# Optimization experiments

Hardware: AMD Instinct MI355X
Metric: run time of the kernel (lower is better)

The kernel has to match this reference:

```python
import jax, jax.numpy as jnp
import numpy as np

N_NODES = 100000
N_EDGES = 1600000
N_GRAPHS = 64
IN_DIM = 397


def setup_inputs() -> dict:
    key = jax.random.key(0)
    ks = jax.random.split(key, 16)
    x = jax.random.normal(ks[0], (N_NODES, IN_DIM), dtype=jnp.float32)
    edge_index = jax.random.randint(ks[1], (2, N_EDGES), 0, N_NODES, dtype=jnp.int64)
    batch = jnp.sort(jax.random.randint(ks[2], (N_NODES,), 0, N_GRAPHS, dtype=jnp.int64))

    def lin(k, fan_in, fan_out):
        s = 1.0 / np.sqrt(fan_in)
        return jax.random.uniform(k, (fan_in, fan_out), jnp.float32, -s, s)

    return {
        "x": x, "edge_index": edge_index, "batch": batch,
        "W1": lin(ks[3], IN_DIM, 128), "b1": jnp.zeros((128,), jnp.float32),
        "W2": lin(ks[4], 128, 128),   "b2": jnp.zeros((128,), jnp.float32),
        "W3": lin(ks[5], 128, 64),    "b3": jnp.zeros((64,), jnp.float32),
        "Wh1": lin(ks[6], 64, 32),    "bh1": jnp.zeros((32,), jnp.float32),
        "Wh2": lin(ks[7], 32, 1),     "bh2": jnp.zeros((1,), jnp.float32),
    }


def _gcn_conv(x, src, dst, deg_isqrt, W, b, n_nodes):
    # PyG GCNConv: linear first, then sym-normalized aggregation with self-loops.
    xw = x @ W  # [N, out]
    norm = deg_isqrt[src] * deg_isqrt[dst]  # [E]
    agg = jax.ops.segment_sum(xw[src] * norm[:, None], dst, num_segments=n_nodes)
    # self-loop contribution: deg^{-1/2}[i] * deg^{-1/2}[i] * xw[i]
    agg = agg + xw * (deg_isqrt * deg_isqrt)[:, None]
    return agg + b


def reference(x, edge_index, batch, W1, b1, W2, b2, W3, b3, Wh1, bh1, Wh2, bh2):
    n_nodes = x.shape[0]
    src, dst = edge_index[0], edge_index[1]
    # degree after adding self-loops (edge weight 1), counted at destination
    deg = jax.ops.segment_sum(jnp.ones_like(src, dtype=x.dtype), dst,
                              num_segments=n_nodes) + 1.0
    deg_isqrt = jax.lax.rsqrt(deg)

    h = jax.nn.relu(_gcn_conv(x, src, dst, deg_isqrt, W1, b1, n_nodes))
    # dropout p=0.2 -> identity in eval
    h = jax.nn.relu(_gcn_conv(h, src, dst, deg_isqrt, W2, b2, n_nodes))
    h = jax.nn.relu(_gcn_conv(h, src, dst, deg_isqrt, W3, b3, n_nodes))

    # global max pool over graphs in the batch
    g = jax.ops.segment_max(h, batch, num_segments=N_GRAPHS)  # [G, 64]

    # MLP head (Dropout(0.3) identity in eval)
    g = jax.nn.relu(g @ Wh1 + bh1)
    out = g @ Wh2 + bh2  # [G, 1]
    return out.squeeze(-1)
```

## Files before the change

kernel.cpp:

```cpp
#include <hip/hip_runtime.h>
#include <hip/hip_bf16.h>
#include <hip/hip_fp16.h>


typedef float f4u __attribute__((ext_vector_type(4), aligned(4)));
typedef unsigned short u16;
typedef u16 u16x8 __attribute__((ext_vector_type(8)));
typedef short bf16x8 __attribute__((ext_vector_type(8)));
typedef float f32x4 __attribute__((ext_vector_type(4)));
typedef _Float16 f16;
typedef f16 f16x8 __attribute__((ext_vector_type(8)));

__device__ __forceinline__ u16 bf16_rne(float f) {
    unsigned u = __float_as_uint(f);
    return (u16)((u + 0x7FFF + ((u >> 16) & 1)) >> 16);
}
__device__ __forceinline__ float bf16_f(u16 h) {
    return __uint_as_float(((unsigned)h) << 16);
}

__global__ void deg_count_kernel(const int* __restrict__ ei, int* __restrict__ cnt, int E) {
    int e = blockIdx.x * 256 + threadIdx.x;
    if (e < E) atomicAdd(&cnt[ei[E + e]], 1);
}

__global__ void deg_fin_kernel(const int* __restrict__ cnt, float* __restrict__ disq, int N) {
    int i = blockIdx.x * 256 + threadIdx.x;
    if (i < N) disq[i] = rsqrtf((float)cnt[i] + 1.0f);
}

__global__ void scan_pass1(const int* __restrict__ cnt, int* __restrict__ bsum, int N) {
    __shared__ int s[256];
    int t = threadIdx.x;
    int base = blockIdx.x * 1024 + t * 4;
    int sum = 0;
    #pragma unroll
    for (int j = 0; j < 4; ++j) { int idx = base + j; if (idx < N) sum += cnt[idx]; }
    s[t] = sum; __syncthreads();
    for (int off = 128; off; off >>= 1) {
        if (t < off) s[t] += s[t + off];
        __syncthreads();
    }
    if (t == 0) bsum[blockIdx.x] = s[0];
}

__global__ void scan_pass2(const int* __restrict__ bsum, int* __restrict__ boff,
                           int nchunks, int* __restrict__ rp, int N, int E) {
    __shared__ int s[256];
    int t = threadIdx.x;
    int v = (t < nchunks) ? bsum[t] : 0;
    s[t] = v; __syncthreads();
    for (int off = 1; off < 256; off <<= 1) {
        int x = (t >= off) ? s[t - off] : 0;
        __syncthreads();
        s[t] += x;
        __syncthreads();
    }
    boff[t] = s[t] - v;
    if (t == 0) rp[N] = E;
}

__global__ void scan_pass3(const int* __restrict__ cnt, const int* __restrict__ boff,
                           int* __restrict__ rp, int N) {
    __shared__ int s[256];
    int t = threadIdx.x;
    int base = blockIdx.x * 1024 + t * 4;
    int v[4]; int sum = 0;
    #pragma unroll
    for (int j = 0; j < 4; ++j) { int idx = base + j; v[j] = (idx < N) ? cnt[idx] : 0; sum += v[j]; }
    s[t] = sum; __syncthreads();
    for (int off = 1; off < 256; off <<= 1) {
        int x = (t >= off) ? s[t - off] : 0;
        __syncthreads();
        s[t] += x;
        __syncthreads();
    }
    int ex = s[t] - sum + boff[blockIdx.x];
    #pragma unroll
    for (int j = 0; j < 4; ++j) { int idx = base + j; if (idx < N) { rp[idx] = ex; ex += v[j]; } }
}

__global__ void scatter_kernel(const int* __restrict__ ei, const float* __restrict__ disq,
                               const int* __restrict__ rp, int* __restrict__ fill,
                               int2* __restrict__ esw, int E) {
    int e = blockIdx.x * 256 + threadIdx.x;
    if (e >= E) return;
    int s = ei[e];
    int d = ei[E + e];
    int pos = rp[d] + atomicAdd(&fill[d], 1);
    int2 p; p.x = s; p.y = __float_as_int(disq[s] * disq[d]);
    esw[pos] = p;
}

__global__ void cvtw_kernel(const float* __restrict__ W, u16* __restrict__ Wthi,
                            u16* __restrict__ Wtlo, int K, int KP, int BN) {
    int idx = blockIdx.x * 256 + threadIdx.x;
    if (idx >= KP * BN) return;
    int c = idx / KP;
    int k = idx % KP;
    float v = (k < K) ? W[(long)k * BN + c] : 0.f;
    u16 h = bf16_rne(v);
    Wthi[idx] = h;
    Wtlo[idx] = bf16_rne(v - bf16_f(h));
}

template <int BN, bool AFP32>
__global__ __launch_bounds__(512) void mfma_gemm(
    const float* __restrict__ Af, const u16* __restrict__ Ahi,
    const u16* __restrict__ Alo, const u16* __restrict__ Wthi,
    const u16* __restrict__ Wtlo, f16* __restrict__ Xh, int N, int K, int KP)
{
    constexpr int FC = BN / 16;
    __shared__ u16 Wh[BN * 40];
    __shared__ u16 Wl[BN * 40];
    const int tid = threadIdx.x;
    const int w = tid >> 6;
    const int l = tid & 63;
    const int l15 = l & 15;
    const int koff = (l >> 4) * 8;
    const long base = (long)blockIdx.x * 128;
    const long arow = base + w * 16 + l15;
    const bool rowOK = (arow < N);

    f32x4 acc[FC];
    #pragma unroll
    for (int j = 0; j < FC; ++j) acc[j] = (f32x4){0.f, 0.f, 0.f, 0.f};

    for (int k0 = 0; k0 < KP; k0 += 32) {
        {
            int i2 = tid;
            if (i2 < BN * 4) {
                int c = i2 >> 2;
                int kq = (i2 & 3) * 8;
                *(u16x8*)&Wh[c * 40 + kq] = *(const u16x8*)&Wthi[(long)c * KP + k0 + kq];
                *(u16x8*)&Wl[c * 40 + kq] = *(const u16x8*)&Wtlo[(long)c * KP + k0 + kq];
            }
        }
        bf16x8 ah, al;
        {
            u16x8 hv = (u16x8)0, lv = (u16x8)0;
            if constexpr (AFP32) {
                int rem = K - (k0 + koff);
                if (rowOK && rem > 0) {
                    const float* ap = &Af[arow * (long)K + k0 + koff];
                    float f[8];
                    if (rem >= 8) {
                        f4u v0 = *(const f4u*)ap;
                        f4u v1 = *(const f4u*)(ap + 4);
                        f[0] = v0.x; f[1] = v0.y; f[2] = v0.z; f[3] = v0.w;
                        f[4] = v1.x; f[5] = v1.y; f[6] = v1.z; f[7] = v1.w;
                    } else {
                        #pragma unroll
                        for (int j = 0; j < 8; ++j) f[j] = (j < rem) ? ap[j] : 0.f;
                    }
                    #pragma unroll
                    for (int j = 0; j < 8; ++j) {
                        u16 h = bf16_rne(f[j]);
                        hv[j] = h;
                        lv[j] = bf16_rne(f[j] - bf16_f(h));
                    }
                }
            } else {
                if (rowOK) {
                    hv = *(const u16x8*)&Ahi[arow * (long)K + k0 + koff];
                    lv = *(const u16x8*)&Alo[arow * (long)K + k0 + koff];
                }
            }
            ah = __builtin_bit_cast(bf16x8, hv);
            al = __builtin_bit_cast(bf16x8, lv);
        }
        __syncthreads();
        #pragma unroll
        for (int fc = 0; fc < FC; ++fc) {
            int wr = (fc * 16 + l15) * 40 + koff;
            bf16x8 bh = *(const bf16x8*)&Wh[wr];
            bf16x8 bl = *(const bf16x8*)&Wl[wr];
            acc[fc] = __builtin_amdgcn_mfma_f32_16x16x32_bf16(ah, bh, acc[fc], 0, 0, 0);
            acc[fc] = __builtin_amdgcn_mfma_f32_16x16x32_bf16(al, bh, acc[fc], 0, 0, 0);
            acc[fc] = __builtin_amdgcn_mfma_f32_16x16x32_bf16(ah, bl, acc[fc], 0, 0, 0);
        }
        __syncthreads();
    }
    #pragma unroll
    for (int fc = 0; fc < FC; ++fc) {
        int col = fc * 16 + l15;
        #pragma unroll
        for (int reg = 0; reg < 4; ++reg) {
            long row = base + w * 16 + (l >> 4) * 4 + reg;
            if (row < N) Xh[row * BN + col] = (f16)acc[fc][reg];
        }
    }
}

template <int C, bool B16OUT>
__global__ __launch_bounds__(256) void agg_kernel(
    const f16* __restrict__ xh, const float* __restrict__ disq,
    const int* __restrict__ rp, const int2* __restrict__ esw,
    const float* __restrict__ bias, float* __restrict__ h,
    u16* __restrict__ hhi, u16* __restrict__ hlo, int N)
{
    int i = blockIdx.x * 4 + (threadIdx.x >> 6);
    if (i >= N) return;
    int lane = threadIdx.x & 63;
    int e0 = rp[i], e1 = rp[i + 1];
    constexpr int LPE = C / 8;
    constexpr int EPW = 64 / LPE;
    int sub = lane / LPE;
    int col = lane % LPE;
    const f16x8* x8 = (const f16x8*)xh;

    float a0[8], a1[8];
    #pragma unroll
    for (int j = 0; j < 8; ++j) { a0[j] = 0.f; a1[j] = 0.f; }

    int e = e0 + sub;
    for (; e + EPW < e1; e += 2 * EPW) {
        int2 p0 = esw[e];
        int2 p1 = esw[e + EPW];
        f16x8 v0 = x8[(long)p0.x * LPE + col];
        f16x8 v1 = x8[(long)p1.x * LPE + col];
        float w0 = __int_as_float(p0.y), w1 = __int_as_float(p1.y);
        #pragma unroll
        for (int j = 0; j < 8; ++j) {
            a0[j] += (float)v0[j] * w0;
            a1[j] += (float)v1[j] * w1;
        }
    }
    for (; e < e1; e += EPW) {
        int2 p0 = esw[e];
        f16x8 v0 = x8[(long)p0.x * LPE + col];
        float w0 = __int_as_float(p0.y);
        #pragma unroll
        for (int j = 0; j < 8; ++j) a0[j] += (float)v0[j] * w0;
    }
    #pragma unroll
    for (int j = 0; j < 8; ++j) a0[j] += a1[j];
    #pragma unroll
    for (int m = LPE; m < 64; m <<= 1) {
        #pragma unroll
        for (int j = 0; j < 8; ++j) a0[j] += __shfl_xor(a0[j], m, 64);
    }
    if (sub == 0) {
        float ds = disq[i];
        float ws = ds * ds;
        f16x8 v = x8[(long)i * LPE + col];
        const float* bp = bias + col * 8;
        float4 b0 = *(const float4*)bp;
        float4 b1 = *(const float4*)(bp + 4);
        float bb[8] = {b0.x, b0.y, b0.z, b0.w, b1.x, b1.y, b1.z, b1.w};
        float o[8];
        #pragma unroll
        for (int j = 0; j < 8; ++j)
            o[j] = fmaxf(a0[j] + (float)v[j] * ws + bb[j], 0.f);
        if constexpr (B16OUT) {
            u16x8 oh, ol;
            #pragma unroll
            for (int j = 0; j < 8; ++j) {
                u16 hh = bf16_rne(o[j]);
                oh[j] = hh;
                ol[j] = bf16_rne(o[j] - bf16_f(hh));
            }
            *(u16x8*)&hhi[(long)i * C + col * 8] = oh;
            *(u16x8*)&hlo[(long)i * C + col * 8] = ol;
        } else {
            float4 v0 = {o[0], o[1], o[2], o[3]};
            float4 v1 = {o[4], o[5], o[6], o[7]};
            *(float4*)&h[(long)i * C + col * 8] = v0;
            *(float4*)&h[(long)i * C + col * 8 + 4] = v1;
        }
    }
}

__global__ __launch_bounds__(256) void pool_kernel(
    const float* __restrict__ h, const int* __restrict__ batch,
    float* __restrict__ g, int N)
{
    int c = threadIdx.x & 63;
    int slot = threadIdx.x >> 6;
    int base = blockIdx.x * 512;
    int end = base + 512; if (end > N) end = N;
    int cur = -1; float m = 0.f;
    for (int n = base + slot; n < end; n += 4) {
        int b = batch[n];
        float v = h[(long)n * 64 + c];
        if (b != cur) {
            if (cur >= 0) atomicMax((int*)&g[cur * 64 + c], __float_as_int(m));
            cur = b; m = v;
        } else {
            m = fmaxf(m, v);
        }
    }
    if (cur >= 0) atomicMax((int*)&g[cur * 64 + c], __float_as_int(m));
}

__global__ void head_kernel(const float* __restrict__ g, const float* __restrict__ Wh1,
                            const float* __restrict__ bh1, const float* __restrict__ Wh2,
                            const float* __restrict__ bh2, float* __restrict__ out, int G) {
    int r = threadIdx.x;
    if (r >= G) return;
    float hid[32];
    #pragma unroll
    for (int j = 0; j < 32; ++j) {
        float s = bh1[j];
        for (int k = 0; k < 64; ++k) s += g[r * 64 + k] * Wh1[k * 32 + j];
        hid[j] = fmaxf(s, 0.f);
    }
    float o = bh2[0];
    #pragma unroll
    for (int j = 0; j < 32; ++j) o += hid[j] * Wh2[j];
    out[r] = o;
}

extern "C" void kernel_launch(void* const* d_in, const int* in_sizes, int n_in,
                              void* d_out, int out_size, void* d_ws, size_t ws_size,
                              hipStream_t stream) {
    const float* x   = (const float*)d_in[0];
    const int*   ei  = (const int*)d_in[1];
    const int*   bat = (const int*)d_in[2];
    const float* W1  = (const float*)d_in[3];
    const float* b1  = (const float*)d_in[4];
    const float* W2  = (const float*)d_in[5];
    const float* b2  = (const float*)d_in[6];
    const float* W3  = (const float*)d_in[7];
    const float* b3  = (const float*)d_in[8];
    const float* Wh1 = (const float*)d_in[9];
    const float* bh1 = (const float*)d_in[10];
    const float* Wh2 = (const float*)d_in[11];
    const float* bh2 = (const float*)d_in[12];
    float* out = (float*)d_out;

    const int N = in_sizes[2];
    const int E = in_sizes[1] / 2;
    const int K1 = in_sizes[0] / N;
    const int G = out_size;
    const int KP1 = ((K1 + 31) / 32) * 32;

    char* wsp = (char*)d_ws;
    size_t off = 0;
    auto alloc = [&](size_t bytes) -> void* {
        void* p = wsp + off;
        off = (off + bytes + 255) & ~(size_t)255;
        return p;
    };
    int*   cnt   = (int*)alloc((size_t)N * 4);
    float* disq  = (float*)alloc((size_t)N * 4);
    int*   rp    = (int*)alloc((size_t)(N + 1) * 4);
    int*   bsum  = (int*)alloc(256 * 4);
    int*   boff  = (int*)alloc(256 * 4);
    int2*  esw   = (int2*)alloc((size_t)E * 8);
    u16*   Wt1hi = (u16*)alloc((size_t)KP1 * 128 * 2);
    u16*   Wt1lo = (u16*)alloc((size_t)KP1 * 128 * 2);
    u16*   Wt2hi = (u16*)alloc((size_t)128 * 128 * 2);
    u16*   Wt2lo = (u16*)alloc((size_t)128 * 128 * 2);
    u16*   Wt3hi = (u16*)alloc((size_t)128 * 64 * 2);
    u16*   Wt3lo = (u16*)alloc((size_t)128 * 64 * 2);
    f16*   Xh    = (f16*)alloc((size_t)N * 128 * 2);
    u16*   Hhi   = (u16*)alloc((size_t)N * 128 * 2);
    u16*   Hlo   = (u16*)alloc((size_t)N * 128 * 2);
    float* h3    = (float*)alloc((size_t)N * 64 * 4);
    float* g     = (float*)alloc((size_t)G * 64 * 4);

    const int nchunks = (N + 1023) / 1024;

    (void)hipMemsetAsync(cnt, 0, (size_t)N * 4, stream);
    deg_count_kernel<<<(E + 255) / 256, 256, 0, stream>>>(ei, cnt, E);
    deg_fin_kernel<<<(N + 255) / 256, 256, 0, stream>>>(cnt, disq, N);
    scan_pass1<<<nchunks, 256, 0, stream>>>(cnt, bsum, N);
    scan_pass2<<<1, 256, 0, stream>>>(bsum, boff, nchunks, rp, N, E);
    scan_pass3<<<nchunks, 256, 0, stream>>>(cnt, boff, rp, N);
    (void)hipMemsetAsync(cnt, 0, (size_t)N * 4, stream);
    scatter_kernel<<<(E + 255) / 256, 256, 0, stream>>>(ei, disq, rp, cnt, esw, E);

    cvtw_kernel<<<(KP1 * 128 + 255) / 256, 256, 0, stream>>>(W1, Wt1hi, Wt1lo, K1, KP1, 128);
    cvtw_kernel<<<(128 * 128 + 255) / 256, 256, 0, stream>>>(W2, Wt2hi, Wt2lo, 128, 128, 128);
    cvtw_kernel<<<(128 * 64 + 255) / 256, 256, 0, stream>>>(W3, Wt3hi, Wt3lo, 128, 128, 64);

    int gblocks = (N + 127) / 128;
    int ablocks = (N + 3) / 4;
    mfma_gemm<128, true><<<gblocks, 512, 0, stream>>>(x, nullptr, nullptr, Wt1hi, Wt1lo, Xh, N, K1, KP1);
    agg_kernel<128, true><<<ablocks, 256, 0, stream>>>(Xh, disq, rp, esw, b1, nullptr, Hhi, Hlo, N);
    mfma_gemm<128, false><<<gblocks, 512, 0, stream>>>(nullptr, Hhi, Hlo, Wt2hi, Wt2lo, Xh, N, 128, 128);
    agg_kernel<128, true><<<ablocks, 256, 0, stream>>>(Xh, disq, rp, esw, b2, nullptr, Hhi, Hlo, N);
    mfma_gemm<64, false><<<gblocks, 512, 0, stream>>>(nullptr, Hhi, Hlo, Wt3hi, Wt3lo, Xh, N, 128, 128);
    agg_kernel<64, false><<<ablocks, 256, 0, stream>>>(Xh, disq, rp, esw, b3, h3, nullptr, nullptr, N);
    (void)hipMemsetAsync(g, 0, (size_t)G * 64 * 4, stream);
    pool_kernel<<<(N + 511) / 512, 256, 0, stream>>>(h3, bat, g, N);
    head_kernel<<<1, 64, 0, stream>>>(g, Wh1, bh1, Wh2, bh2, out, G);
}
```

Baseline: 531.4 us.

## Retile MFMA GEMM to 64x32 per-wave tiles with weights read directly from global

Reworks the bf16x3 MFMA GEMM so each wave computes a 64-row by 32-column tile (4x2 fragments) instead of 16 rows by all columns. Weight fragments are loaded straight from global memory/cache into registers, and the shared-memory staging and both __syncthreads per K step are removed. The aim is to reuse each A fragment across two column fragments and each W fragment across four row fragments, and to drop the barrier stalls. In exchange, A rows are reread by several column-waves (BN=128 uses 4 waves per row block), register pressure goes up, and block size and grid change.

```diff
diff --git a/kernel.cpp b/kernel.cpp
--- a/kernel.cpp
+++ b/kernel.cpp
@@ -105,44 +105,46 @@
 }
 
 template <int BN, bool AFP32>
-__global__ __launch_bounds__(512) void mfma_gemm(
+__global__ __launch_bounds__(256) void mfma_gemm(
     const float* __restrict__ Af, const u16* __restrict__ Ahi,
     const u16* __restrict__ Alo, const u16* __restrict__ Wthi,
     const u16* __restrict__ Wtlo, f16* __restrict__ Xh, int N, int K, int KP)
 {
-    constexpr int FC = BN / 16;
-    __shared__ u16 Wh[BN * 40];
-    __shared__ u16 Wl[BN * 40];
+    constexpr int WCOL = BN / 32;
+    constexpr int BM = 64 * (4 / WCOL);
     const int tid = threadIdx.x;
     const int w = tid >> 6;
     const int l = tid & 63;
     const int l15 = l & 15;
     const int koff = (l >> 4) * 8;
-    const long base = (long)blockIdx.x * 128;
-    const long arow = base + w * 16 + l15;
-    const bool rowOK = (arow < N);
-
-    f32x4 acc[FC];
-    #pragma unroll
-    for (int j = 0; j < FC; ++j) acc[j] = (f32x4){0.f, 0.f, 0.f, 0.f};
-
+    const int cw = w % WCOL;
+    const int rw = w / WCOL;
+    const long base = (long)blockIdx.x * BM + rw * 64;
+
+    f32x4 acc[4][2];
+    #pragma unroll
+    for (int i = 0; i < 4; ++i)
+        #pragma unroll
+        for (int j = 0; j < 2; ++j) acc[i][j] = (f32x4){0.f, 0.f, 0.f, 0.f};
+
+    #pragma unroll 2
     for (int k0 = 0; k0 < KP; k0 += 32) {
-        {
-            int i2 = tid;
-            if (i2 < BN * 4) {
-                int c = i2 >> 2;
-                int kq = (i2 & 3) * 8;
-                *(u16x8*)&Wh[c * 40 + kq] = *(const u16x8*)&Wthi[(long)c * KP + k0 + kq];
-                *(u16x8*)&Wl[c * 40 + kq] = *(const u16x8*)&Wtlo[(long)c * KP + k0 + kq];
-            }
-        }
-        bf16x8 ah, al;
-        {
+        bf16x8 bh[2], bl[2];
+        #pragma unroll
+        for (int fc = 0; fc < 2; ++fc) {
+            long wr = (long)(cw * 32 + fc * 16 + l15) * KP + k0 + koff;
+            bh[fc] = __builtin_bit_cast(bf16x8, *(const u16x8*)(Wthi + wr));
+            bl[fc] = __builtin_bit_cast(bf16x8, *(const u16x8*)(Wtlo + wr));
+        }
+        bf16x8 ah[4], al[4];
+        #pragma unroll
+        for (int fr = 0; fr < 4; ++fr) {
+            long row = base + fr * 16 + l15;
             u16x8 hv = (u16x8)0, lv = (u16x8)0;
             if constexpr (AFP32) {
                 int rem = K - (k0 + koff);
-                if (rowOK && rem > 0) {
-                    const float* ap = &Af[arow * (long)K + k0 + koff];
+                if (row < N && rem > 0) {
+                    const float* ap = &Af[row * (long)K + k0 + koff];
                     float f[8];
                     if (rem >= 8) {
                         f4u v0 = *(const f4u*)ap;
@@ -161,33 +163,34 @@
                     }
                 }
             } else {
-                if (rowOK) {
-                    hv = *(const u16x8*)&Ahi[arow * (long)K + k0 + koff];
-                    lv = *(const u16x8*)&Alo[arow * (long)K + k0 + koff];
+                if (row < N) {
+                    hv = *(const u16x8*)&Ahi[row * (long)K + k0 + koff];
+                    lv = *(const u16x8*)&Alo[row * (long)K + k0 + koff];
                 }
             }
-            ah = __builtin_bit_cast(bf16x8, hv);
-            al = __builtin_bit_cast(bf16x8, lv);
-        }
-        __syncthreads();
-        #pragma unroll
-        for (int fc = 0; fc < FC; ++fc) {
-            int wr = (fc * 16 + l15) * 40 + koff;
-            bf16x8 bh = *(const bf16x8*)&Wh[wr];
-            bf16x8 bl = *(const bf16x8*)&Wl[wr];
-            acc[fc] = __builtin_amdgcn_mfma_f32_16x16x32_bf16(ah, bh, acc[fc], 0, 0, 0);
-            acc[fc] = __builtin_amdgcn_mfma_f32_16x16x32_bf16(al, bh, acc[fc], 0, 0, 0);
-            acc[fc] = __builtin_amdgcn_mfma_f32_16x16x32_bf16(ah, bl, acc[fc], 0, 0, 0);
-        }
-        __syncthreads();
-    }
-    #pragma unroll
-    for (int fc = 0; fc < FC; ++fc) {
-        int col = fc * 16 + l15;
-        #pragma unroll
-        for (int reg = 0; reg < 4; ++reg) {
-            long row = base + w * 16 + (l >> 4) * 4 + reg;
-            if (row < N) Xh[row * BN + col] = (f16)acc[fc][reg];
+            ah[fr] = __builtin_bit_cast(bf16x8, hv);
+            al[fr] = __builtin_bit_cast(bf16x8, lv);
+        }
+        #pragma unroll
+        for (int fr = 0; fr < 4; ++fr) {
+            #pragma unroll
+            for (int fc = 0; fc < 2; ++fc) {
+                acc[fr][fc] = __builtin_amdgcn_mfma_f32_16x16x32_bf16(ah[fr], bh[fc], acc[fr][fc], 0, 0, 0);
+                acc[fr][fc] = __builtin_amdgcn_mfma_f32_16x16x32_bf16(al[fr], bh[fc], acc[fr][fc], 0, 0, 0);
+                acc[fr][fc] = __builtin_amdgcn_mfma_f32_16x16x32_bf16(ah[fr], bl[fc], acc[fr][fc], 0, 0, 0);
+            }
+        }
+    }
+    #pragma unroll
+    for (int fr = 0; fr < 4; ++fr) {
+        #pragma unroll
+        for (int fc = 0; fc < 2; ++fc) {
+            int col = cw * 32 + fc * 16 + l15;
+            #pragma unroll
+            for (int reg = 0; reg < 4; ++reg) {
+                long row = base + fr * 16 + (l >> 4) * 4 + reg;
+                if (row < N) Xh[row * BN + col] = (f16)acc[fr][fc][reg];
+            }
         }
     }
 }
@@ -375,13 +378,14 @@
     cvtw_kernel<<<(128 * 128 + 255) / 256, 256, 0, stream>>>(W2, Wt2hi, Wt2lo, 128, 128, 128);
     cvtw_kernel<<<(128 * 64 + 255) / 256, 256, 0, stream>>>(W3, Wt3hi, Wt3lo, 128, 128, 64);
 
-    int gblocks = (N + 127) / 128;
+    int g128 = (N + 63) / 64;
+    int g64  = (N + 127) / 128;
     int ablocks = (N + 3) / 4;
-    mfma_gemm<128, true><<<gblocks, 512, 0, stream>>>(x, nullptr, nullptr, Wt1hi, Wt1lo, Xh, N, K1, KP1);
+    mfma_gemm<128, true><<<g128, 256, 0, stream>>>(x, nullptr, nullptr, Wt1hi, Wt1lo, Xh, N, K1, KP1);
     agg_kernel<128, true><<<ablocks, 256, 0, stream>>>(Xh, disq, rp, esw, b1, nullptr, Hhi, Hlo, N);
-    mfma_gemm<128, false><<<gblocks, 512, 0, stream>>>(nullptr, Hhi, Hlo, Wt2hi, Wt2lo, Xh, N, 128, 128);
+    mfma_gemm<128, false><<<g128, 256, 0, stream>>>(nullptr, Hhi, Hlo, Wt2hi, Wt2lo, Xh, N, 128, 128);
     agg_kernel<128, true><<<ablocks, 256, 0, stream>>>(Xh, disq, rp, esw, b2, nullptr, Hhi, Hlo, N);
-    mfma_gemm<64, false><<<gblocks, 512, 0, stream>>>(nullptr, Hhi, Hlo, Wt3hi, Wt3lo, Xh, N, 128, 128);
+    mfma_gemm<64, false><<<g64, 256, 0, stream>>>(nullptr, Hhi, Hlo, Wt3hi, Wt3lo, Xh, N, 128, 128);
     agg_kernel<64, false><<<ablocks, 256, 0, stream>>>(Xh, disq, rp, esw, b3, h3, nullptr, nullptr, N);
     (void)hipMemsetAsync(g, 0, (size_t)G * 64 * 4, stream);
     pool_kernel<<<(N + 511) / 512, 256, 0, stream>>>(h3, bat, g, N);
```

Result: slower. 607.5 us (+14.3%).
